# Kernel tuning notes

Hardware: AMD Instinct MI355X
Metric: run time of the kernel (lower is better)

Reference implementation:

```python
import jax, jax.numpy as jnp
import numpy as np

C, H, W_DIM, B, N = 9, 260, 346, 16, 32768
E = B * N
HIDDEN = 100
NEG_SLOPE = 0.1


def setup_inputs() -> dict:
    key = jax.random.key(0)
    ks = jax.random.split(key, 10)
    xs = jax.random.randint(ks[0], (E,), 0, W_DIM, dtype=jnp.int32)
    ys = jax.random.randint(ks[1], (E,), 0, H, dtype=jnp.int32)
    ts = jax.random.uniform(ks[2], (E,), dtype=jnp.float32)
    ps = jax.random.randint(ks[3], (E,), 0, 2, dtype=jnp.int32)  # polarity already mapped to {0,1}
    bs = jnp.repeat(jnp.arange(B, dtype=jnp.int32), N)           # batch id per event
    W1 = jax.random.normal(ks[4], (HIDDEN, 1), dtype=jnp.float32) * 0.5
    b1 = jax.random.normal(ks[5], (HIDDEN,), dtype=jnp.float32) * 0.1
    W2 = jax.random.normal(ks[6], (HIDDEN, HIDDEN), dtype=jnp.float32) * 0.1
    b2 = jax.random.normal(ks[7], (HIDDEN,), dtype=jnp.float32) * 0.1
    W3 = jax.random.normal(ks[8], (1, HIDDEN), dtype=jnp.float32) * 0.1
    b3 = jax.random.normal(ks[9], (1,), dtype=jnp.float32) * 0.1
    return {"xs": xs, "ys": ys, "ts": ts, "ps": ps, "bs": bs,
            "W1": W1, "b1": b1, "W2": W2, "b2": b2, "W3": W3, "b3": b3}


def _lrelu(v):
    return jnp.where(v >= 0, v, NEG_SLOPE * v)


def _value_layer(t, W1, b1, W2, b2, W3, b3):
    # ValueLayer MLP: scalar per event -> hidden -> hidden -> scalar
    h = _lrelu(t[:, None] * W1[:, 0][None, :] + b1)  # [E, HIDDEN]
    h = _lrelu(h @ W2.T + b2)                        # [E, HIDDEN]
    return (h @ W3.T + b3)[:, 0]                     # [E]


def reference(xs, ys, ts, ps, bs, W1, b1, W2, b2, W3, b3):
    num_voxels = 2 * C * H * W_DIM * B
    # idx = x + W*y + W*H*C*p + W*H*C*2*b  (+ W*H*i_bin per bin)
    idx0 = xs + W_DIM * ys + (W_DIM * H * C) * ps + (2 * W_DIM * H * C) * bs
    vox = jnp.zeros((num_voxels,), dtype=ts.dtype)
    for i_bin in range(C):  # fixed small loop over temporal bins
        vals = ts * _value_layer(ts - i_bin / (C - 1), W1, b1, W2, b2, W3, b3)
        idx = jnp.clip(idx0 + (W_DIM * H) * i_bin, 0, num_voxels - 1)
        vox = vox.at[idx].add(vals)
    vox = vox.reshape(B, 2, C, H, W_DIM)
    # concat polarity channels -> [B, 2C, H, W]
    return jnp.concatenate([vox[:, 0], vox[:, 1]], axis=1)
```

## Files before the change

### kernel.cpp

```cpp
#include <hip/hip_runtime.h>

#define C_BINS 9
#define H_DIM 260
#define WDIM 346
#define B_DIM 16
#define N_PER_B 32768
#define HIDDEN 100
#define NEG_SLOPE 0.1f
#define WH (WDIM * H_DIM)
#define NUM_VOXELS (2 * C_BINS * WH * B_DIM)
#define TABLE_N 16384
#define HALF_N (TABLE_N / 2)
#define BIN_SHIFT (TABLE_N / 16)
#define T9_STRIDE 12

#define ROWS_PER_TILE 5
#define TILES_PER_BP 52
#define LBUCKETS (2 * TILES_PER_BP)
#define NBUCKETS (B_DIM * LBUCKETS)
#define BUCKET_CAP 512
#define EV_PER_BLOCK 1024
#define TILE_ELEMS (C_BINS * ROWS_PER_TILE * WDIM)
#define ROW_F2 (ROWS_PER_TILE * WDIM / 2)

#define WS_TABLE_OFF 0
#define WS_COUNT_OFF 66048
#define WS_T9_OFF    73728
#define WS_REC_OFF   467968
#define WS_REC_SZ    ((size_t)NBUCKETS * BUCKET_CAP * 8)
#define WS_NEEDED    (WS_REC_OFF + WS_REC_SZ)

__global__ __launch_bounds__(256) void build_table_kernel(
    const float* __restrict__ W1, const float* __restrict__ b1,
    const float* __restrict__ W2, const float* __restrict__ b2,
    const float* __restrict__ W3, const float* __restrict__ b3,
    float* __restrict__ table, float* __restrict__ t9,
    unsigned int* __restrict__ counts, int write_t9)
{
    __shared__ __align__(16) float sW2[HIDDEN * HIDDEN + 8];
    __shared__ float sW1[HIDDEN], sb1[HIDDEN], sb2[HIDDEN], sW3[HIDDEN];
    const int tid = threadIdx.x;

    if (write_t9 && blockIdx.x == 0) {
        for (int i = tid; i < NBUCKETS; i += 256) counts[i] = 0u;
    }

    {
        const float4* __restrict__ src = (const float4*)W2;
        float4* dst = (float4*)sW2;
        for (int i = tid; i < (HIDDEN * HIDDEN) / 4; i += 256) dst[i] = src[i];
    }
    if (tid < 8) sW2[HIDDEN * HIDDEN + tid] = 0.0f;
    if (tid < HIDDEN) {
        sW1[tid] = W1[tid];
        sb1[tid] = b1[tid];
        sb2[tid] = b2[tid];
        sW3[tid] = W3[tid];
    }
    __syncthreads();

    const int entry_local = tid >> 3;
    const int o  = tid & 7;
    const int q  = o & 3;
    const int j0 = (o >> 2) * 52;
    const int g  = blockIdx.x * 32 + entry_local;
    if (g > TABLE_N) return;
    const float u = -1.0f + (2.0f / (float)TABLE_N) * (float)g;

    float h1[52];
#pragma unroll
    for (int j = 0; j < 52; ++j) {
        const int jj = j0 + j;
        float v = (jj < HIDDEN) ? fmaf(u, sW1[jj], sb1[jj]) : 0.0f;
        h1[j] = (v >= 0.0f) ? v : NEG_SLOPE * v;
    }

    float acc = 0.0f;
    for (int k = q; k < HIDDEN; k += 4) {
        const float* __restrict__ row = &sW2[k * HIDDEN + j0];
        float a0 = 0.f, a1 = 0.f, a2 = 0.f, a3 = 0.f;
#pragma unroll
        for (int j = 0; j < 52; j += 4) {
            a0 = fmaf(row[j + 0], h1[j + 0], a0);
            a1 = fmaf(row[j + 1], h1[j + 1], a1);
            a2 = fmaf(row[j + 2], h1[j + 2], a2);
            a3 = fmaf(row[j + 3], h1[j + 3], a3);
        }
        float part = (a0 + a1) + (a2 + a3);
        part += __shfl_xor(part, 4);
        float a = sb2[k] + part;
        a = (a >= 0.0f) ? a : NEG_SLOPE * a;
        acc = fmaf(a, sW3[k], acc);
    }
    acc += __shfl_xor(acc, 1);
    acc += __shfl_xor(acc, 2);
    if (o == 0) {
        const float val = acc + b3[0];
        table[g] = val;
        if (write_t9) {
#pragma unroll
            for (int i = 0; i < C_BINS; ++i) {
                const int r = g - HALF_N + BIN_SHIFT * i;
                if (r >= 0 && r <= HALF_N) t9[r * T9_STRIDE + i] = val;
            }
        }
    }
}

__global__ __launch_bounds__(256) void bucket_kernel(
    const int* __restrict__ xs, const int* __restrict__ ys,
    const float* __restrict__ ts, const int* __restrict__ ps,
    unsigned int* __restrict__ counts,
    unsigned long long* __restrict__ records, int E)
{
    __shared__ unsigned lcnt[LBUCKETS];
    __shared__ unsigned lpre[LBUCKETS];
    __shared__ unsigned gbase[LBUCKETS];
    __shared__ unsigned scan[2][128];
    __shared__ unsigned long long stage[EV_PER_BLOCK];
    __shared__ unsigned char slb[EV_PER_BLOCK];

    const int tid = threadIdx.x;
    const int e0  = blockIdx.x * EV_PER_BLOCK;
    const int b   = e0 >> 15;

    for (int i = tid; i < LBUCKETS; i += 256) lcnt[i] = 0;
    __syncthreads();

    int lb[4];
    unsigned rank[4];
    unsigned long long rec[4];
    const int eb = e0 + tid * 4;
    if (eb + 3 < E) {
        const int v4 = (e0 >> 2) + tid;
        const int4   xv = ((const int4*)xs)[v4];
        const int4   yv = ((const int4*)ys)[v4];
        const int4   pv = ((const int4*)ps)[v4];
        const float4 tv = ((const float4*)ts)[v4];
        const int   xa[4] = {xv.x, xv.y, xv.z, xv.w};
        const int   ya[4] = {yv.x, yv.y, yv.z, yv.w};
        const int   pa[4] = {pv.x, pv.y, pv.z, pv.w};
        const float ta[4] = {tv.x, tv.y, tv.z, tv.w};
#pragma unroll
        for (int j = 0; j < 4; ++j) {
            const int yt = ya[j] / ROWS_PER_TILE;
            const int yl = ya[j] - yt * ROWS_PER_TILE;
            lb[j]  = pa[j] * TILES_PER_BP + yt;
            rec[j] = ((unsigned long long)__float_as_uint(ta[j]) << 32)
                   | (unsigned)(yl * WDIM + xa[j]);
            rank[j] = atomicAdd(&lcnt[lb[j]], 1u);
        }
    } else {
#pragma unroll
        for (int j = 0; j < 4; ++j) {
            const int e = eb + j;
            if (e < E) {
                const int   x = xs[e];
                const int   y = ys[e];
                const int   p = ps[e];
                const float t = ts[e];
                const int  yt = y / ROWS_PER_TILE;
                const int  yl = y - yt * ROWS_PER_TILE;
                lb[j]  = p * TILES_PER_BP + yt;
                rec[j] = ((unsigned long long)__float_as_uint(t) << 32)
                       | (unsigned)(yl * WDIM + x);
                rank[j] = atomicAdd(&lcnt[lb[j]], 1u);
            } else {
                lb[j] = -1;
            }
        }
    }
    __syncthreads();

    if (tid < 128) scan[0][tid] = (tid < LBUCKETS) ? lcnt[tid] : 0u;
    __syncthreads();
    int src = 0;
    for (int off = 1; off < 128; off <<= 1) {
        if (tid < 128) {
            unsigned v = scan[src][tid];
            if (tid >= off) v += scan[src][tid - off];
            scan[src ^ 1][tid] = v;
        }
        src ^= 1;
        __syncthreads();
    }
    if (tid < LBUCKETS) {
        const unsigned c = lcnt[tid];
        lpre[tid]  = scan[src][tid] - c;
        gbase[tid] = c ? atomicAdd(&counts[b * LBUCKETS + tid], c) : 0u;
    }
    __syncthreads();

#pragma unroll
    for (int j = 0; j < 4; ++j) {
        if (lb[j] >= 0) {
            const unsigned s = lpre[lb[j]] + rank[j];
            stage[s] = rec[j];
            slb[s]   = (unsigned char)lb[j];
        }
    }
    __syncthreads();

    const int nblk = (E - e0 < EV_PER_BLOCK) ? (E - e0) : EV_PER_BLOCK;
    for (int s = tid; s < nblk; s += 256) {
        const int l = slb[s];
        const unsigned ofs = gbase[l] + ((unsigned)s - lpre[l]);
        if (ofs < BUCKET_CAP)
            records[(size_t)(b * LBUCKETS + l) * BUCKET_CAP + ofs] = stage[s];
    }
}

__global__ __launch_bounds__(512) void tile_kernel(
    const unsigned int* __restrict__ counts, const uint2* __restrict__ records,
    const float* __restrict__ t9, float* __restrict__ out)
{
    __shared__ float tile[TILE_ELEMS];
    const int tid = threadIdx.x;
    const int bucket = blockIdx.x;
    const int yt = bucket % TILES_PER_BP;
    const int bp = bucket / TILES_PER_BP;

    const int n = min(counts[bucket], (unsigned)BUCKET_CAP);
    const uint2* __restrict__ rec = records + (size_t)bucket * BUCKET_CAP;

    {
        float2* __restrict__ t2 = (float2*)tile;
        const float2 z = {0.f, 0.f};
        for (int k = tid; k < TILE_ELEMS / 2; k += 512) t2[k] = z;
    }
    __syncthreads();

    for (int r = tid; r < n; r += 512) {
        const uint2 v = rec[r];
        const int   pix = (int)v.x;
        const float t   = __uint_as_float(v.y);
        const float pos = (t + 1.0f) * ((float)TABLE_N * 0.5f);
        const int   i0  = (int)pos;
        const float frac = pos - (float)i0;
        const int   rr  = i0 - HALF_N;
        const float4* __restrict__ rowp = (const float4*)(t9 + rr * T9_STRIDE);
        const float4 a0 = rowp[0], a1 = rowp[1], a2 = rowp[2];
        const float4 c0 = rowp[3], c1 = rowp[4], c2 = rowp[5];
        const float t0v[9] = {a0.x, a0.y, a0.z, a0.w, a1.x, a1.y, a1.z, a1.w, a2.x};
        const float t1v[9] = {c0.x, c0.y, c0.z, c0.w, c1.x, c1.y, c1.z, c1.w, c2.x};
#pragma unroll
        for (int i = 0; i < C_BINS; ++i) {
            const float val = t * fmaf(frac, t1v[i] - t0v[i], t0v[i]);
            atomicAdd(&tile[i * (ROWS_PER_TILE * WDIM) + pix], val);
        }
    }
    __syncthreads();

    float* __restrict__ obase = out + (size_t)bp * (C_BINS * WH) + yt * (ROWS_PER_TILE * WDIM);
#pragma unroll
    for (int i = 0; i < C_BINS; ++i) {
        const float2* __restrict__ s2 = (const float2*)&tile[i * (ROWS_PER_TILE * WDIM)];
        float2* __restrict__ d2 = (float2*)(obase + i * WH);
        for (int k = tid; k < ROW_F2; k += 512) d2[k] = s2[k];
    }
}

__global__ __launch_bounds__(256) void zero_kernel(float4* __restrict__ out, int n4)
{
    int i = blockIdx.x * 256 + threadIdx.x;
    int stride = gridDim.x * 256;
    float4 z = {0.f, 0.f, 0.f, 0.f};
    for (; i < n4; i += stride) out[i] = z;
}

__global__ __launch_bounds__(256) void scatter_kernel(
    const int* __restrict__ xs, const int* __restrict__ ys,
    const float* __restrict__ ts, const int* __restrict__ ps,
    const int* __restrict__ bs, const float* __restrict__ table,
    float* __restrict__ out, int E)
{
    const int e = blockIdx.x * 256 + threadIdx.x;
    if (e >= E) return;
    const int x = xs[e], y = ys[e], p = ps[e], b = bs[e];
    const float t = ts[e];
    int idx0 = x + WDIM * y + (WH * C_BINS) * p + (2 * WH * C_BINS) * b;
#pragma unroll
    for (int i = 0; i < C_BINS; ++i) {
        float u   = t - (float)i * (1.0f / (float)(C_BINS - 1));
        float pos = (u + 1.0f) * ((float)TABLE_N * 0.5f);
        int   i0  = (int)pos;
        i0 = (i0 < 0) ? 0 : ((i0 > TABLE_N - 1) ? TABLE_N - 1 : i0);
        float frac = pos - (float)i0;
        float f  = fmaf(frac, table[i0 + 1] - table[i0], table[i0]);
        int idx = idx0 + WH * i;
        idx = (idx < 0) ? 0 : ((idx >= NUM_VOXELS) ? NUM_VOXELS - 1 : idx);
        atomicAdd(&out[idx], t * f);
    }
}

extern "C" void kernel_launch(void* const* d_in, const int* in_sizes, int n_in,
                              void* d_out, int out_size, void* d_ws, size_t ws_size,
                              hipStream_t stream)
{
    const int*   xs = (const int*)d_in[0];
    const int*   ys = (const int*)d_in[1];
    const float* ts = (const float*)d_in[2];
    const int*   ps = (const int*)d_in[3];
    const int*   bs = (const int*)d_in[4];
    const float* W1 = (const float*)d_in[5];
    const float* b1 = (const float*)d_in[6];
    const float* W2 = (const float*)d_in[7];
    const float* b2 = (const float*)d_in[8];
    const float* W3 = (const float*)d_in[9];
    const float* b3 = (const float*)d_in[10];

    float* out = (float*)d_out;
    char*  ws  = (char*)d_ws;
    float* table = (float*)(ws + WS_TABLE_OFF);
    unsigned int* counts = (unsigned int*)(ws + WS_COUNT_OFF);
    float* t9 = (float*)(ws + WS_T9_OFF);
    const int E = in_sizes[0];
    const int use_fast = (ws_size >= WS_NEEDED) ? 1 : 0;

    build_table_kernel<<<(TABLE_N / 32) + 1, 256, 0, stream>>>(
        W1, b1, W2, b2, W3, b3, table, t9, counts, use_fast);

    if (use_fast) {
        unsigned long long* records = (unsigned long long*)(ws + WS_REC_OFF);
        bucket_kernel<<<(E + EV_PER_BLOCK - 1) / EV_PER_BLOCK, 256, 0, stream>>>(
            xs, ys, ts, ps, counts, records, E);
        tile_kernel<<<NBUCKETS, 512, 0, stream>>>(
            counts, (const uint2*)records, t9, out);
    } else {
        zero_kernel<<<1024, 256, 0, stream>>>((float4*)out, out_size / 4);
        scatter_kernel<<<(E + 255) / 256, 256, 0, stream>>>(
            xs, ys, ts, ps, bs, table, out, E);
    }
}
```

Before: 182.2 us.

## Fuse table build and event bucketing into one launch; use 4-row tiles

Merges the MLP lookup-table build and the event bucketing into a single kernel whose block range is split between the two jobs, so they run concurrently instead of back to back. The counter zeroing moves to a memset. Tiles shrink from 5 to 4 rows so the bucket index becomes a shift/mask instead of a division, and tile zeroing and write-out use float4 accesses. The cost is more buckets and tile-kernel blocks, plus a larger shared-memory footprint for the fused kernel, which may lower occupancy for the bucketing blocks.

```diff
diff --git a/kernel.cpp b/kernel.cpp
--- a/kernel.cpp
+++ b/kernel.cpp
@@ -14,199 +14,206 @@
 #define BIN_SHIFT (TABLE_N / 16)
 #define T9_STRIDE 12
 
-#define ROWS_PER_TILE 5
-#define TILES_PER_BP 52
+#define ROWS_PER_TILE 4
+#define TILES_PER_BP 65
 #define LBUCKETS (2 * TILES_PER_BP)
 #define NBUCKETS (B_DIM * LBUCKETS)
 #define BUCKET_CAP 512
 #define EV_PER_BLOCK 1024
 #define TILE_ELEMS (C_BINS * ROWS_PER_TILE * WDIM)
-#define ROW_F2 (ROWS_PER_TILE * WDIM / 2)
+#define TILE_F4 (TILE_ELEMS / 4)
+#define CHUNK_F4 (ROWS_PER_TILE * WDIM / 4)
+#define BUILD_BLOCKS (TABLE_N / 32 + 1)
+
+#define SMEM_BYTES 41632
+#define SM_STAGE 0
+#define SM_SCAN  8192
+#define SM_LCNT  10240
+#define SM_LPRE  10760
+#define SM_GBASE 11280
+#define SM_SLB   11800
 
 #define WS_TABLE_OFF 0
 #define WS_COUNT_OFF 66048
-#define WS_T9_OFF    73728
-#define WS_REC_OFF   467968
+#define WS_T9_OFF    74752
+#define WS_REC_OFF   468480
 #define WS_REC_SZ    ((size_t)NBUCKETS * BUCKET_CAP * 8)
 #define WS_NEEDED    (WS_REC_OFF + WS_REC_SZ)
 
-__global__ __launch_bounds__(256) void build_table_kernel(
+__global__ __launch_bounds__(256) void fused_build_bucket_kernel(
+    const int* __restrict__ xs, const int* __restrict__ ys,
+    const float* __restrict__ ts, const int* __restrict__ ps,
     const float* __restrict__ W1, const float* __restrict__ b1,
     const float* __restrict__ W2, const float* __restrict__ b2,
     const float* __restrict__ W3, const float* __restrict__ b3,
     float* __restrict__ table, float* __restrict__ t9,
-    unsigned int* __restrict__ counts, int write_t9)
-{
-    __shared__ __align__(16) float sW2[HIDDEN * HIDDEN + 8];
-    __shared__ float sW1[HIDDEN], sb1[HIDDEN], sb2[HIDDEN], sW3[HIDDEN];
+    unsigned int* __restrict__ counts,
+    unsigned long long* __restrict__ records,
+    int E, int n_bucket_blocks, int write_t9)
+{
+    __shared__ __align__(16) char smem[SMEM_BYTES];
     const int tid = threadIdx.x;
 
-    if (write_t9 && blockIdx.x == 0) {
-        for (int i = tid; i < NBUCKETS; i += 256) counts[i] = 0u;
-    }
-
-    {
-        const float4* __restrict__ src = (const float4*)W2;
-        float4* dst = (float4*)sW2;
-        for (int i = tid; i < (HIDDEN * HIDDEN) / 4; i += 256) dst[i] = src[i];
-    }
-    if (tid < 8) sW2[HIDDEN * HIDDEN + tid] = 0.0f;
-    if (tid < HIDDEN) {
-        sW1[tid] = W1[tid];
-        sb1[tid] = b1[tid];
-        sb2[tid] = b2[tid];
-        sW3[tid] = W3[tid];
-    }
-    __syncthreads();
-
-    const int entry_local = tid >> 3;
-    const int o  = tid & 7;
-    const int q  = o & 3;
-    const int j0 = (o >> 2) * 52;
-    const int g  = blockIdx.x * 32 + entry_local;
-    if (g > TABLE_N) return;
-    const float u = -1.0f + (2.0f / (float)TABLE_N) * (float)g;
-
-    float h1[52];
-#pragma unroll
-    for (int j = 0; j < 52; ++j) {
-        const int jj = j0 + j;
-        float v = (jj < HIDDEN) ? fmaf(u, sW1[jj], sb1[jj]) : 0.0f;
-        h1[j] = (v >= 0.0f) ? v : NEG_SLOPE * v;
-    }
-
-    float acc = 0.0f;
-    for (int k = q; k < HIDDEN; k += 4) {
-        const float* __restrict__ row = &sW2[k * HIDDEN + j0];
-        float a0 = 0.f, a1 = 0.f, a2 = 0.f, a3 = 0.f;
-#pragma unroll
-        for (int j = 0; j < 52; j += 4) {
-            a0 = fmaf(row[j + 0], h1[j + 0], a0);
-            a1 = fmaf(row[j + 1], h1[j + 1], a1);
-            a2 = fmaf(row[j + 2], h1[j + 2], a2);
-            a3 = fmaf(row[j + 3], h1[j + 3], a3);
-        }
-        float part = (a0 + a1) + (a2 + a3);
-        part += __shfl_xor(part, 4);
-        float a = sb2[k] + part;
-        a = (a >= 0.0f) ? a : NEG_SLOPE * a;
-        acc = fmaf(a, sW3[k], acc);
-    }
-    acc += __shfl_xor(acc, 1);
-    acc += __shfl_xor(acc, 2);
-    if (o == 0) {
-        const float val = acc + b3[0];
-        table[g] = val;
-        if (write_t9) {
-#pragma unroll
-            for (int i = 0; i < C_BINS; ++i) {
-                const int r = g - HALF_N + BIN_SHIFT * i;
-                if (r >= 0 && r <= HALF_N) t9[r * T9_STRIDE + i] = val;
-            }
-        }
-    }
-}
-
-__global__ __launch_bounds__(256) void bucket_kernel(
-    const int* __restrict__ xs, const int* __restrict__ ys,
-    const float* __restrict__ ts, const int* __restrict__ ps,
-    unsigned int* __restrict__ counts,
-    unsigned long long* __restrict__ records, int E)
-{
-    __shared__ unsigned lcnt[LBUCKETS];
-    __shared__ unsigned lpre[LBUCKETS];
-    __shared__ unsigned gbase[LBUCKETS];
-    __shared__ unsigned scan[2][128];
-    __shared__ unsigned long long stage[EV_PER_BLOCK];
-    __shared__ unsigned char slb[EV_PER_BLOCK];
-
-    const int tid = threadIdx.x;
-    const int e0  = blockIdx.x * EV_PER_BLOCK;
-    const int b   = e0 >> 15;
-
-    for (int i = tid; i < LBUCKETS; i += 256) lcnt[i] = 0;
-    __syncthreads();
-
-    int lb[4];
-    unsigned rank[4];
-    unsigned long long rec[4];
-    const int eb = e0 + tid * 4;
-    if (eb + 3 < E) {
-        const int v4 = (e0 >> 2) + tid;
-        const int4   xv = ((const int4*)xs)[v4];
-        const int4   yv = ((const int4*)ys)[v4];
-        const int4   pv = ((const int4*)ps)[v4];
-        const float4 tv = ((const float4*)ts)[v4];
-        const int   xa[4] = {xv.x, xv.y, xv.z, xv.w};
-        const int   ya[4] = {yv.x, yv.y, yv.z, yv.w};
-        const int   pa[4] = {pv.x, pv.y, pv.z, pv.w};
-        const float ta[4] = {tv.x, tv.y, tv.z, tv.w};
+    if (blockIdx.x < (unsigned)n_bucket_blocks) {
+        unsigned long long* stage = (unsigned long long*)(smem + SM_STAGE);
+        unsigned*      scan  = (unsigned*)(smem + SM_SCAN);
+        unsigned*      lcnt  = (unsigned*)(smem + SM_LCNT);
+        unsigned*      lpre  = (unsigned*)(smem + SM_LPRE);
+        unsigned*      gbase = (unsigned*)(smem + SM_GBASE);
+        unsigned char* slb   = (unsigned char*)(smem + SM_SLB);
+
+        const int e0 = blockIdx.x * EV_PER_BLOCK;
+        const int b  = e0 >> 15;
+
+        for (int i = tid; i < LBUCKETS; i += 256) lcnt[i] = 0;
+        __syncthreads();
+
+        int lb[4];
+        unsigned rank[4];
+        unsigned long long rec[4];
+        const int eb = e0 + tid * 4;
+        if (eb + 3 < E) {
+            const int v4 = (e0 >> 2) + tid;
+            const int4   xv = ((const int4*)xs)[v4];
+            const int4   yv = ((const int4*)ys)[v4];
+            const int4   pv = ((const int4*)ps)[v4];
+            const float4 tv = ((const float4*)ts)[v4];
+            const int   xa[4] = {xv.x, xv.y, xv.z, xv.w};
+            const int   ya[4] = {yv.x, yv.y, yv.z, yv.w};
+            const int   pa[4] = {pv.x, pv.y, pv.z, pv.w};
+            const float ta[4] = {tv.x, tv.y, tv.z, tv.w};
+#pragma unroll
+            for (int j = 0; j < 4; ++j) {
+                const int yt = ya[j] >> 2;
+                const int yl = ya[j] & 3;
+                lb[j]  = pa[j] * TILES_PER_BP + yt;
+                rec[j] = ((unsigned long long)__float_as_uint(ta[j]) << 32)
+                       | (unsigned)(yl * WDIM + xa[j]);
+                rank[j] = atomicAdd(&lcnt[lb[j]], 1u);
+            }
+        } else {
+#pragma unroll
+            for (int j = 0; j < 4; ++j) {
+                const int e = eb + j;
+                if (e < E) {
+                    const int   x = xs[e];
+                    const int   y = ys[e];
+                    const int   p = ps[e];
+                    const float t = ts[e];
+                    const int  yt = y >> 2;
+                    const int  yl = y & 3;
+                    lb[j]  = p * TILES_PER_BP + yt;
+                    rec[j] = ((unsigned long long)__float_as_uint(t) << 32)
+                           | (unsigned)(yl * WDIM + x);
+                    rank[j] = atomicAdd(&lcnt[lb[j]], 1u);
+                } else {
+                    lb[j] = -1;
+                }
+            }
+        }
+        __syncthreads();
+
+        scan[tid] = (tid < LBUCKETS) ? lcnt[tid] : 0u;
+        __syncthreads();
+        int src = 0;
+        for (int off = 1; off < 256; off <<= 1) {
+            unsigned v = scan[src * 256 + tid];
+            if (tid >= off) v += scan[src * 256 + tid - off];
+            scan[(src ^ 1) * 256 + tid] = v;
+            src ^= 1;
+            __syncthreads();
+        }
+        if (tid < LBUCKETS) {
+            const unsigned c = lcnt[tid];
+            lpre[tid]  = scan[src * 256 + tid] - c;
+            gbase[tid] = c ? atomicAdd(&counts[b * LBUCKETS + tid], c) : 0u;
+        }
+        __syncthreads();
+
 #pragma unroll
         for (int j = 0; j < 4; ++j) {
-            const int yt = ya[j] / ROWS_PER_TILE;
-            const int yl = ya[j] - yt * ROWS_PER_TILE;
-            lb[j]  = pa[j] * TILES_PER_BP + yt;
-            rec[j] = ((unsigned long long)__float_as_uint(ta[j]) << 32)
-                   | (unsigned)(yl * WDIM + xa[j]);
-            rank[j] = atomicAdd(&lcnt[lb[j]], 1u);
+            if (lb[j] >= 0) {
+                const unsigned s = lpre[lb[j]] + rank[j];
+                stage[s] = rec[j];
+                slb[s]   = (unsigned char)lb[j];
+            }
+        }
+        __syncthreads();
+
+        const int nblk = (E - e0 < EV_PER_BLOCK) ? (E - e0) : EV_PER_BLOCK;
+        for (int s = tid; s < nblk; s += 256) {
+            const int l = slb[s];
+            const unsigned ofs = gbase[l] + ((unsigned)s - lpre[l]);
+            if (ofs < BUCKET_CAP)
+                records[(size_t)(b * LBUCKETS + l) * BUCKET_CAP + ofs] = stage[s];
         }
     } else {
-#pragma unroll
-        for (int j = 0; j < 4; ++j) {
-            const int e = eb + j;
-            if (e < E) {
-                const int   x = xs[e];
-                const int   y = ys[e];
-                const int   p = ps[e];
-                const float t = ts[e];
-                const int  yt = y / ROWS_PER_TILE;
-                const int  yl = y - yt * ROWS_PER_TILE;
-                lb[j]  = p * TILES_PER_BP + yt;
-                rec[j] = ((unsigned long long)__float_as_uint(t) << 32)
-                       | (unsigned)(yl * WDIM + x);
-                rank[j] = atomicAdd(&lcnt[lb[j]], 1u);
-            } else {
-                lb[j] = -1;
-            }
-        }
-    }
-    __syncthreads();
-
-    if (tid < 128) scan[0][tid] = (tid < LBUCKETS) ? lcnt[tid] : 0u;
-    __syncthreads();
-    int src = 0;
-    for (int off = 1; off < 128; off <<= 1) {
-        if (tid < 128) {
-            unsigned v = scan[src][tid];
-            if (tid >= off) v += scan[src][tid - off];
-            scan[src ^ 1][tid] = v;
-        }
-        src ^= 1;
-        __syncthreads();
-    }
-    if (tid < LBUCKETS) {
-        const unsigned c = lcnt[tid];
-        lpre[tid]  = scan[src][tid] - c;
-        gbase[tid] = c ? atomicAdd(&counts[b * LBUCKETS + tid], c) : 0u;
-    }
-    __syncthreads();
-
-#pragma unroll
-    for (int j = 0; j < 4; ++j) {
-        if (lb[j] >= 0) {
-            const unsigned s = lpre[lb[j]] + rank[j];
-            stage[s] = rec[j];
-            slb[s]   = (unsigned char)lb[j];
-        }
-    }
-    __syncthreads();
-
-    const int nblk = (E - e0 < EV_PER_BLOCK) ? (E - e0) : EV_PER_BLOCK;
-    for (int s = tid; s < nblk; s += 256) {
-        const int l = slb[s];
-        const unsigned ofs = gbase[l] + ((unsigned)s - lpre[l]);
-        if (ofs < BUCKET_CAP)
-            records[(size_t)(b * LBUCKETS + l) * BUCKET_CAP + ofs] = stage[s];
+        float* sW2 = (float*)smem;
+        float* sW1 = (float*)(smem + 40032);
+        float* sb1 = sW1 + HIDDEN;
+        float* sb2 = sb1 + HIDDEN;
+        float* sW3 = sb2 + HIDDEN;
+
+        {
+            const float4* __restrict__ srcw = (const float4*)W2;
+            float4* dst = (float4*)sW2;
+            for (int i = tid; i < (HIDDEN * HIDDEN) / 4; i += 256) dst[i] = srcw[i];
+        }
+        if (tid < 8) sW2[HIDDEN * HIDDEN + tid] = 0.0f;
+        if (tid < HIDDEN) {
+            sW1[tid] = W1[tid];
+            sb1[tid] = b1[tid];
+            sb2[tid] = b2[tid];
+            sW3[tid] = W3[tid];
+        }
+        __syncthreads();
+
+        const int entry_local = tid >> 3;
+        const int o  = tid & 7;
+        const int q  = o & 3;
+        const int j0 = (o >> 2) * 52;
+        const int g  = (blockIdx.x - n_bucket_blocks) * 32 + entry_local;
+        if (g > TABLE_N) return;
+        const float u = -1.0f + (2.0f / (float)TABLE_N) * (float)g;
+
+        float h1[52];
+#pragma unroll
+        for (int j = 0; j < 52; ++j) {
+            const int jj = j0 + j;
+            float v = (jj < HIDDEN) ? fmaf(u, sW1[jj], sb1[jj]) : 0.0f;
+            h1[j] = (v >= 0.0f) ? v : NEG_SLOPE * v;
+        }
+
+        float acc = 0.0f;
+        for (int k = q; k < HIDDEN; k += 4) {
+            const float* __restrict__ row = &sW2[k * HIDDEN + j0];
+            float a0 = 0.f, a1 = 0.f, a2 = 0.f, a3 = 0.f;
+#pragma unroll
+            for (int j = 0; j < 52; j += 4) {
+                a0 = fmaf(row[j + 0], h1[j + 0], a0);
+                a1 = fmaf(row[j + 1], h1[j + 1], a1);
+                a2 = fmaf(row[j + 2], h1[j + 2], a2);
+                a3 = fmaf(row[j + 3], h1[j + 3], a3);
+            }
+            float part = (a0 + a1) + (a2 + a3);
+            part += __shfl_xor(part, 4);
+            float a = sb2[k] + part;
+            a = (a >= 0.0f) ? a : NEG_SLOPE * a;
+            acc = fmaf(a, sW3[k], acc);
+        }
+        acc += __shfl_xor(acc, 1);
+        acc += __shfl_xor(acc, 2);
+        if (o == 0) {
+            const float val = acc + b3[0];
+            table[g] = val;
+            if (write_t9) {
+#pragma unroll
+                for (int i = 0; i < C_BINS; ++i) {
+                    const int r = g - HALF_N + BIN_SHIFT * i;
+                    if (r >= 0 && r <= HALF_N) t9[r * T9_STRIDE + i] = val;
+                }
+            }
+        }
     }
 }
 
@@ -214,7 +221,7 @@
     const unsigned int* __restrict__ counts, const uint2* __restrict__ records,
     const float* __restrict__ t9, float* __restrict__ out)
 {
-    __shared__ float tile[TILE_ELEMS];
+    __shared__ __align__(16) float tile[TILE_ELEMS];
     const int tid = threadIdx.x;
     const int bucket = blockIdx.x;
     const int yt = bucket % TILES_PER_BP;
@@ -223,10 +230,10 @@
     const int n = min(counts[bucket], (unsigned)BUCKET_CAP);
     const uint2* __restrict__ rec = records + (size_t)bucket * BUCKET_CAP;
 
+    float4* __restrict__ t4 = (float4*)tile;
     {
-        float2* __restrict__ t2 = (float2*)tile;
-        const float2 z = {0.f, 0.f};
-        for (int k = tid; k < TILE_ELEMS / 2; k += 512) t2[k] = z;
+        const float4 z = {0.f, 0.f, 0.f, 0.f};
+        for (int k = tid; k < TILE_F4; k += 512) t4[k] = z;
     }
     __syncthreads();
 
@@ -251,12 +258,12 @@
     }
     __syncthreads();
 
-    float* __restrict__ obase = out + (size_t)bp * (C_BINS * WH) + yt * (ROWS_PER_TILE * WDIM);
-#pragma unroll
-    for (int i = 0; i < C_BINS; ++i) {
-        const float2* __restrict__ s2 = (const float2*)&tile[i * (ROWS_PER_TILE * WDIM)];
-        float2* __restrict__ d2 = (float2*)(obase + i * WH);
-        for (int k = tid; k < ROW_F2; k += 512) d2[k] = s2[k];
+    float* __restrict__ obase = out + (size_t)bp * (C_BINS * WH)
+                              + yt * (ROWS_PER_TILE * WDIM);
+    for (int s = tid; s < TILE_F4; s += 512) {
+        const int i = s / CHUNK_F4;
+        const int k = s - i * CHUNK_F4;
+        ((float4*)(obase + i * WH))[k] = t4[i * CHUNK_F4 + k];
     }
 }
 
@@ -317,16 +324,19 @@
     const int E = in_sizes[0];
     const int use_fast = (ws_size >= WS_NEEDED) ? 1 : 0;
 
-    build_table_kernel<<<(TABLE_N / 32) + 1, 256, 0, stream>>>(
-        W1, b1, W2, b2, W3, b3, table, t9, counts, use_fast);
-
     if (use_fast) {
         unsigned long long* records = (unsigned long long*)(ws + WS_REC_OFF);
-        bucket_kernel<<<(E + EV_PER_BLOCK - 1) / EV_PER_BLOCK, 256, 0, stream>>>(
-            xs, ys, ts, ps, counts, records, E);
+        const int nbB = (E + EV_PER_BLOCK - 1) / EV_PER_BLOCK;
+        hipMemsetAsync(counts, 0, NBUCKETS * sizeof(unsigned int), stream);
+        fused_build_bucket_kernel<<<nbB + BUILD_BLOCKS, 256, 0, stream>>>(
+            xs, ys, ts, ps, W1, b1, W2, b2, W3, b3,
+            table, t9, counts, records, E, nbB, 1);
         tile_kernel<<<NBUCKETS, 512, 0, stream>>>(
             counts, (const uint2*)records, t9, out);
     } else {
+        fused_build_bucket_kernel<<<BUILD_BLOCKS, 256, 0, stream>>>(
+            xs, ys, ts, ps, W1, b1, W2, b2, W3, b3,
+            table, t9, counts, (unsigned long long*)out , E, 0, 0);
         zero_kernel<<<1024, 256, 0, stream>>>((float4*)out, out_size / 4);
         scatter_kernel<<<(E + 255) / 256, 256, 0, stream>>>(
             xs, ys, ts, ps, bs, table, out, E);
```

Result: faster. 172.7 us (-5.2%).
